# Performance work log

Hardware: AMD Instinct MI355X
Metric: run time of the kernel (lower is better)

The kernel has to match this reference:

```python
import jax, jax.numpy as jnp
import numpy as np

HIDDEN = 1024
HEADS = 16
HEAD_DIM = HIDDEN // HEADS


def setup_inputs() -> dict:
    key = jax.random.key(0)
    k_x, k_wa, k_ba, k_wp, k_bp = jax.random.split(key, 5)
    x = jax.random.normal(k_x, (2, 2048, HIDDEN), dtype=jnp.float32)
    s_a = 1.0 / np.sqrt(HIDDEN)
    # torch Linear default init ~ U(-1/sqrt(fan_in), 1/sqrt(fan_in)); stored as [in, out]
    W_attn = jax.random.uniform(k_wa, (HIDDEN, 3 * HIDDEN), jnp.float32, -s_a, s_a)
    b_attn = jax.random.uniform(k_ba, (3 * HIDDEN,), jnp.float32, -s_a, s_a)
    W_proj = jax.random.uniform(k_wp, (HIDDEN, HIDDEN), jnp.float32, -s_a, s_a)
    b_proj = jax.random.uniform(k_bp, (HIDDEN,), jnp.float32, -s_a, s_a)
    return {"x": x, "W_attn": W_attn, "b_attn": b_attn, "W_proj": W_proj, "b_proj": b_proj}


def reference(x, W_attn, b_attn, W_proj, b_proj):
    B, S, D = x.shape
    H, Hd = HEADS, HEAD_DIM
    qkv = x @ W_attn + b_attn                     # [B, S, 3D]
    q, k, v = jnp.split(qkv, 3, axis=-1)
    # [B, H, S, Hd]
    q = q.reshape(B, S, H, Hd).transpose(0, 2, 1, 3)
    k = k.reshape(B, S, H, Hd).transpose(0, 2, 1, 3)
    v = v.reshape(B, S, H, Hd).transpose(0, 2, 1, 3)
    scale = 1.0 / np.sqrt(Hd).astype(np.float32)
    scores = jnp.einsum('bhqd,bhkd->bhqk', q, k) * scale   # [B, H, S, S]
    causal = jnp.triu(jnp.ones((S, S), dtype=bool), k=1)   # True above diagonal
    scores = jnp.where(causal, -jnp.inf, scores)
    probs = jax.nn.softmax(scores, axis=-1)
    # dropout p=0.0 -> identity (eval-mode equivalent)
    ctx = jnp.einsum('bhqk,bhkd->bhqd', probs, v)           # [B, H, S, Hd]
    ctx = ctx.transpose(0, 2, 1, 3).reshape(B, S, D)
    return ctx @ W_proj + b_proj
```

## Files before the change

### kernel.cpp

```cpp
#include <hip/hip_runtime.h>
#include <hip/hip_bf16.h>
#include <stdint.h>

#define HID 1024
#define NH 16
#define HD 64
#define SEQ 2048
#define BATCH 2
#define M_TOT 4096
#define QSCALE 0.18033688011112042f

typedef __attribute__((ext_vector_type(8))) short short8;
typedef __attribute__((ext_vector_type(4))) float f32x4;
typedef __attribute__((ext_vector_type(16))) float f32x16;
typedef __hip_bfloat16 bf16;

__device__ __forceinline__ void load_lds16(const void* g, void* l) {
  __builtin_amdgcn_global_load_lds(
      (const __attribute__((address_space(1))) unsigned int*)g,
      (__attribute__((address_space(3))) unsigned int*)l, 16, 0, 0);
}

__device__ __forceinline__ unsigned short f2bf_bits(float f) {
  __hip_bfloat16 h = __float2bfloat16(f);
  return *reinterpret_cast<unsigned short*>(&h);
}
__device__ __forceinline__ unsigned pack2bf(float a, float b) {
  return (unsigned)f2bf_bits(a) | ((unsigned)f2bf_bits(b) << 16);
}
__device__ __forceinline__ unsigned cvt_pk_bf16(float a, float b) {
  unsigned r;
  asm("v_cvt_pk_bf16_f32 %0, %1, %2" : "=v"(r) : "v"(a), "v"(b));
  return r;
}

__global__ void cvt_f32_to_bf16(const float* __restrict__ in,
                                bf16* __restrict__ out, int n4) {
  int i = blockIdx.x * blockDim.x + threadIdx.x;
  if (i >= n4) return;
  float4 v = reinterpret_cast<const float4*>(in)[i];
  ushort4 o;
  o.x = f2bf_bits(v.x); o.y = f2bf_bits(v.y);
  o.z = f2bf_bits(v.z); o.w = f2bf_bits(v.w);
  reinterpret_cast<ushort4*>(out)[i] = o;
}

__global__ void transpose_cvt2(const float* __restrict__ Wa, bf16* __restrict__ WTa,
                               const float* __restrict__ Wp, bf16* __restrict__ WTp) {
  __shared__ float tile[32][33];
  int bx = blockIdx.x;
  const float* W; bf16* WT; int N;
  if (bx < 96) { W = Wa; WT = WTa; N = 3072; }
  else         { W = Wp; WT = WTp; N = 1024; bx -= 96; }
  const int K = 1024;
  int n0 = bx * 32, k0 = blockIdx.y * 32;
  int tx = threadIdx.x, ty = threadIdx.y;
#pragma unroll
  for (int i = 0; i < 32; i += 8)
    tile[ty + i][tx] = W[(size_t)(k0 + ty + i) * N + n0 + tx];
  __syncthreads();
#pragma unroll
  for (int i = 0; i < 32; i += 8)
    WT[(size_t)(n0 + ty + i) * K + k0 + tx] = __float2bfloat16(tile[tx][ty + i]);
}

template <int EPI>
__global__ __launch_bounds__(256, 2)
void gemm128(const bf16* __restrict__ A, const bf16* __restrict__ BT,
             const float* __restrict__ bias,
             bf16* __restrict__ Qo, bf16* __restrict__ Ko, bf16* __restrict__ Vo,
             float* __restrict__ Fo) {
  const int Kdim = 1024;
  __shared__ char smem[65536];
  const int tid = threadIdx.x;
  const int wid = tid >> 6, lane = tid & 63;
  const int m0 = blockIdx.x * 128;
  const int n0 = blockIdx.y * 128;
  const int wrow = (wid >> 1) * 64, wcol = (wid & 1) * 64;

  f32x4 acc[4][4];
#pragma unroll
  for (int rb = 0; rb < 4; ++rb)
#pragma unroll
    for (int cb = 0; cb < 4; ++cb)
      acc[rb][cb] = (f32x4){0.f, 0.f, 0.f, 0.f};

  const int lr = lane >> 3;
  const int cc = lane & 7;
  const int lc = cc * 8;
  const int fr = lane & 15, fk = (lane >> 4) * 8;

  auto stage = [&](int kt) {
    char* nb = smem + (kt & 1) * 32768;
#pragma unroll
    for (int t = 0; t < 4; ++t) {
      int i = wid * 4 + t;
      int row = i * 8 + lr;
      load_lds16(A + (size_t)(m0 + row) * Kdim + kt * 64 + lc, nb + i * 1024);
      load_lds16(BT + (size_t)(n0 + row) * Kdim + kt * 64 + lc,
                 nb + 16384 + i * 1024);
    }
  };

  stage(0);

  for (int kt = 0; kt < Kdim / 64; ++kt) {
    const bf16* As = (const bf16*)(smem + (kt & 1) * 32768);
    const bf16* Bs = As + 8192;

    __builtin_amdgcn_s_barrier();
    __builtin_amdgcn_sched_barrier(0);

    if (kt + 1 < Kdim / 64) {
      stage(kt + 1);
      asm volatile("s_waitcnt vmcnt(8)" ::: "memory");
    } else {
      asm volatile("s_waitcnt vmcnt(0)" ::: "memory");
    }
    __builtin_amdgcn_sched_barrier(0);

    __builtin_amdgcn_s_barrier();
    __builtin_amdgcn_sched_barrier(0);

    short8 af[4][2], bf_[4][2];
#pragma unroll
    for (int rb = 0; rb < 4; ++rb)
#pragma unroll
      for (int kk = 0; kk < 2; ++kk) {
        af[rb][kk] = *(const short8*)&As[(wrow + rb * 16 + fr) * 64 + kk * 32 + fk];
        bf_[rb][kk] = *(const short8*)&Bs[(wcol + rb * 16 + fr) * 64 + kk * 32 + fk];
      }
    __builtin_amdgcn_s_setprio(1);
#pragma unroll
    for (int rb = 0; rb < 4; ++rb)
#pragma unroll
      for (int cb = 0; cb < 4; ++cb)
#pragma unroll
        for (int kk = 0; kk < 2; ++kk)
          acc[rb][cb] = __builtin_amdgcn_mfma_f32_16x16x32_bf16(
              af[rb][kk], bf_[cb][kk], acc[rb][cb], 0, 0, 0);
    __builtin_amdgcn_s_setprio(0);
  }

  const int fg = (lane >> 4) * 4;
  float bv[4];
#pragma unroll
  for (int cb = 0; cb < 4; ++cb) bv[cb] = bias[n0 + wcol + cb * 16 + fr];

  if (EPI == 0) {
    __syncthreads();
    char* ep = smem + wid * 8192;
    const int ncol = n0 + wcol;
    const int part = ncol >> 10;
    const int h = (ncol & 1023) >> 6;
    const int b = m0 >> 11;
    const int s_base = (m0 + wrow) & 2047;
    const size_t hb = (size_t)(b * NH + h);

    if (part < 2) {
      const float qs = (part == 0) ? QSCALE : 1.f;
#pragma unroll
      for (int rb = 0; rb < 4; ++rb)
#pragma unroll
        for (int cb = 0; cb < 4; ++cb)
#pragma unroll
          for (int j = 0; j < 4; ++j) {
            int row = rb * 16 + fg + j;
            int colb = (cb * 16 + fr) * 2;
            *(unsigned short*)(ep + row * 128 + (colb ^ ((row & 7) << 4))) =
                f2bf_bits((acc[rb][cb][j] + bv[cb]) * qs);
          }
      bf16* dst = (part == 0 ? Qo : Ko) + hb * SEQ * HD;
#pragma unroll
      for (int p = 0; p < 8; ++p) {
        int row = p * 8 + lr;
        uint4 v = *(const uint4*)(ep + row * 128 + ((cc * 16) ^ ((row & 7) << 4)));
        *(uint4*)(dst + (size_t)(s_base + row) * HD + cc * 8) = v;
      }
    } else {
#pragma unroll
      for (int rb = 0; rb < 4; ++rb)
#pragma unroll
        for (int cb = 0; cb < 4; ++cb) {
          int cV = cb * 16 + fr;
          int r0 = (rb * 16 + fg) * 2;
          uint2 wv;
          wv.x = pack2bf(acc[rb][cb][0] + bv[cb], acc[rb][cb][1] + bv[cb]);
          wv.y = pack2bf(acc[rb][cb][2] + bv[cb], acc[rb][cb][3] + bv[cb]);
          *(uint2*)(ep + cV * 128 + (r0 ^ ((cV & 7) << 4))) = wv;
        }
      bf16* dstV = Vo + hb * HD * SEQ;
#pragma unroll
      for (int p = 0; p < 8; ++p) {
        int hd = p * 8 + lr;
        uint4 v = *(const uint4*)(ep + hd * 128 + ((cc * 16) ^ ((hd & 7) << 4)));
        *(uint4*)(dstV + (size_t)hd * SEQ + s_base + cc * 8) = v;
      }
    }
  } else {
#pragma unroll
    for (int rb = 0; rb < 4; ++rb) {
      int r0 = m0 + wrow + rb * 16 + fg;
#pragma unroll
      for (int cb = 0; cb < 4; ++cb) {
        int n = n0 + wcol + cb * 16 + fr;
#pragma unroll
        for (int j = 0; j < 4; ++j)
          Fo[(size_t)(r0 + j) * HID + n] = acc[rb][cb][j] + bv[cb];
      }
    }
  }
}

__global__ __launch_bounds__(256, 2)
void attn_kernel(const bf16* __restrict__ Q, const bf16* __restrict__ K,
                 const bf16* __restrict__ VT, bf16* __restrict__ ctx) {
  __shared__ char smem[65536];
  const int tid = threadIdx.x, wid = tid >> 6, lane = tid & 63;
  const int idx = blockIdx.x;
  const int qt = (idx < 256) ? (15 - (idx >> 5)) : ((idx - 256) >> 5);
  const int bh = idx & 31;
  const int b = bh >> 4, h = bh & 15;
  const size_t base = (size_t)bh * SEQ * HD;
  const int q0 = qt * 128 + wid * 32;

  const int fr = lane & 31, hi = lane >> 5;
  const int lr = lane >> 3;
  const int cc = lane & 7;
  const int qg = q0 + fr;
  const int gc = (cc ^ lr) * 8;

  short8 qf[4];
  const bf16* qp = Q + base + (size_t)qg * HD;
#pragma unroll
  for (int kc = 0; kc < 4; ++kc)
    qf[kc] = *(const short8*)(qp + kc * 16 + hi * 8);

  f32x16 oa[2], ob[2];
#pragma unroll
  for (int da = 0; da < 2; ++da)
#pragma unroll
    for (int r = 0; r < 16; ++r) { oa[da][r] = 0.f; ob[da][r] = 0.f; }
  float lpart = 0.f;

  auto stage_pair = [&](int jp) {
    char* nb = smem + (jp & 1) * 32768;
    const int nv = jp * 128;
#pragma unroll
    for (int u = 0; u < 2; ++u)
#pragma unroll
      for (int t = 0; t < 2; ++t) {
        int i = wid * 2 + t;
        load_lds16(K + base + (size_t)(nv + u * 64 + i * 8 + lr) * HD + gc,
                   nb + u * 16384 + i * 1024);
        load_lds16(VT + base + (size_t)(i * 8 + lr) * SEQ + nv + u * 64 + gc,
                   nb + u * 16384 + 8192 + i * 1024);
      }
  };

  auto tile_compute = [&](const char* sb_t, int kv0, f32x16 (&oc)[2]) {
    f32x16 sa[2];
    __builtin_amdgcn_s_setprio(1);
#pragma unroll
    for (int kb = 0; kb < 2; ++kb) {
#pragma unroll
      for (int r = 0; r < 16; ++r) sa[kb][r] = 0.f;
      const int row = kb * 32 + fr;
      const int swz = (row & 7) << 4;
#pragma unroll
      for (int kc = 0; kc < 4; ++kc) {
        short8 kf = *(const short8*)(sb_t + row * 128 + ((kc * 32 + hi * 16) ^ swz));
        sa[kb] = __builtin_amdgcn_mfma_f32_32x32x16_bf16(kf, qf[kc], sa[kb], 0, 0, 0);
      }
    }
    __builtin_amdgcn_s_setprio(0);

    if (kv0 + 63 > q0) {
#pragma unroll
      for (int kb = 0; kb < 2; ++kb)
#pragma unroll
        for (int r = 0; r < 16; ++r) {
          int kvg = kv0 + kb * 32 + (r & 3) + 8 * (r >> 2) + 4 * hi;
          sa[kb][r] = (kvg > qg) ? -1e30f : sa[kb][r];
        }
    }

    float s0 = 0.f, s1 = 0.f, s2 = 0.f, s3 = 0.f;
#pragma unroll
    for (int kb = 0; kb < 2; ++kb)
#pragma unroll
      for (int r = 0; r < 16; ++r) {
        float e = __builtin_exp2f(sa[kb][r]);
        sa[kb][r] = e;
        if ((r & 3) == 0)      s0 += e;
        else if ((r & 3) == 1) s1 += e;
        else if ((r & 3) == 2) s2 += e;
        else                   s3 += e;
      }
    lpart += (s0 + s1) + (s2 + s3);

    unsigned pk[2][8];
#pragma unroll
    for (int kb = 0; kb < 2; ++kb)
#pragma unroll
      for (int i = 0; i < 8; ++i)
        pk[kb][i] = cvt_pk_bf16(sa[kb][2 * i], sa[kb][2 * i + 1]);

    short8 pfr[4];
#pragma unroll
    for (int ks = 0; ks < 4; ++ks) {
      const int kb = ks >> 1, g = (ks & 1) * 4;
      auto r0 = __builtin_amdgcn_permlane32_swap((int)pk[kb][g + 0],
                                                 (int)pk[kb][g + 2], false, false);
      auto r1 = __builtin_amdgcn_permlane32_swap((int)pk[kb][g + 1],
                                                 (int)pk[kb][g + 3], false, false);
      union { unsigned u[4]; short8 s; } pf;
      pf.u[0] = (unsigned)r0[0]; pf.u[1] = (unsigned)r1[0];
      pf.u[2] = (unsigned)r0[1]; pf.u[3] = (unsigned)r1[1];
      pfr[ks] = pf.s;
    }

    __builtin_amdgcn_s_setprio(1);
#pragma unroll
    for (int da = 0; da < 2; ++da) {
      const int row = da * 32 + fr;
      const int swz = (row & 7) << 4;
#pragma unroll
      for (int ks = 0; ks < 4; ++ks) {
        short8 vf = *(const short8*)(sb_t + 8192 + row * 128 +
                                     ((ks * 32 + hi * 16) ^ swz));
        oc[da] = __builtin_amdgcn_mfma_f32_32x32x16_bf16(vf, pfr[ks], oc[da], 0, 0, 0);
      }
    }
    __builtin_amdgcn_s_setprio(0);
  };

  const int npair = qt + 1;

  stage_pair(0);

  for (int j = 0; j < npair; ++j) {
    char* sb = smem + (j & 1) * 32768;

    __builtin_amdgcn_s_barrier();
    __builtin_amdgcn_sched_barrier(0);

    if (j + 1 < npair) {
      stage_pair(j + 1);
      asm volatile("s_waitcnt vmcnt(8)" ::: "memory");
    } else {
      asm volatile("s_waitcnt vmcnt(0)" ::: "memory");
    }
    __builtin_amdgcn_sched_barrier(0);

    __builtin_amdgcn_s_barrier();
    __builtin_amdgcn_sched_barrier(0);

    const int kv0 = j * 128;
    if (kv0 <= q0 + 31)      tile_compute(sb,         kv0,      oa);
    if (kv0 + 64 <= q0 + 31) tile_compute(sb + 16384, kv0 + 64, ob);
  }

  const float lrun = lpart + __shfl_xor(lpart, 32);
  const float inv = 1.f / lrun;
  char* ep = smem + wid * 4096;
#pragma unroll
  for (int da = 0; da < 2; ++da)
#pragma unroll
    for (int rg = 0; rg < 4; ++rg) {
      int d0 = da * 64 + rg * 16 + hi * 8;
      float v0 = (oa[da][rg * 4 + 0] + ob[da][rg * 4 + 0]) * inv;
      float v1 = (oa[da][rg * 4 + 1] + ob[da][rg * 4 + 1]) * inv;
      float v2 = (oa[da][rg * 4 + 2] + ob[da][rg * 4 + 2]) * inv;
      float v3 = (oa[da][rg * 4 + 3] + ob[da][rg * 4 + 3]) * inv;
      uint2 wv; wv.x = pack2bf(v0, v1); wv.y = pack2bf(v2, v3);
      *(uint2*)(ep + fr * 128 + (d0 ^ ((fr & 7) << 4))) = wv;
    }
#pragma unroll
  for (int p = 0; p < 4; ++p) {
    int qr = p * 8 + lr;
    uint4 v = *(const uint4*)(ep + qr * 128 + ((cc * 16) ^ ((qr & 7) << 4)));
    int s = q0 + qr;
    *(uint4*)(ctx + (size_t)(b * SEQ + s) * HID + h * 64 + cc * 8) = v;
  }
}

extern "C" void kernel_launch(void* const* d_in, const int* in_sizes, int n_in,
                              void* d_out, int out_size, void* d_ws, size_t ws_size,
                              hipStream_t stream) {
  const float* x      = (const float*)d_in[0];
  const float* W_attn = (const float*)d_in[1];
  const float* b_attn = (const float*)d_in[2];
  const float* W_proj = (const float*)d_in[3];
  const float* b_proj = (const float*)d_in[4];
  float* out = (float*)d_out;

  char* ws = (char*)d_ws;
  const size_t MB = 1u << 20;
  bf16* xb   = (bf16*)(ws + 0);
  bf16* WTa  = (bf16*)(ws + 8 * MB);
  bf16* WTp  = (bf16*)(ws + 14 * MB);
  bf16* Qw   = (bf16*)(ws + 16 * MB);
  bf16* Kw   = (bf16*)(ws + 24 * MB);
  bf16* VTw  = (bf16*)(ws + 32 * MB);
  bf16* ctxb = (bf16*)(ws + 40 * MB);

  cvt_f32_to_bf16<<<(M_TOT * HID / 4 + 255) / 256, 256, 0, stream>>>(x, xb, M_TOT * HID / 4);
  transpose_cvt2<<<dim3(128, 32), dim3(32, 8), 0, stream>>>(W_attn, WTa, W_proj, WTp);

  gemm128<0><<<dim3(M_TOT / 128, 3 * HID / 128), 256, 0, stream>>>(
      xb, WTa, b_attn, Qw, Kw, VTw, nullptr);

  attn_kernel<<<dim3(512), 256, 0, stream>>>(Qw, Kw, VTw, ctxb);

  gemm128<1><<<dim3(M_TOT / 128, HID / 128), 256, 0, stream>>>(
      ctxb, WTp, b_proj, nullptr, nullptr, nullptr, out);
}
```

Before: 108.6 us.

## Swizzle GEMM LDS tiles and fuse prep kernels into one launch

Applies an XOR swizzle to the chunk positions of the A and B tiles staged in LDS and matches it in the fragment reads, to reduce LDS bank conflicts in the bf16 MFMA GEMMs. It also merges the x conversion and weight transpose-convert kernels into a single launch with a flattened 1D grid, removing one kernel launch. The cost is more index arithmetic per block.

```diff
diff --git a/kernel.cpp b/kernel.cpp
--- a/kernel.cpp
+++ b/kernel.cpp
@@ -34,27 +34,27 @@
   return r;
 }
 
-__global__ void cvt_f32_to_bf16(const float* __restrict__ in,
-                                bf16* __restrict__ out, int n4) {
-  int i = blockIdx.x * blockDim.x + threadIdx.x;
-  if (i >= n4) return;
-  float4 v = reinterpret_cast<const float4*>(in)[i];
-  ushort4 o;
-  o.x = f2bf_bits(v.x); o.y = f2bf_bits(v.y);
-  o.z = f2bf_bits(v.z); o.w = f2bf_bits(v.w);
-  reinterpret_cast<ushort4*>(out)[i] = o;
-}
-
-__global__ void transpose_cvt2(const float* __restrict__ Wa, bf16* __restrict__ WTa,
-                               const float* __restrict__ Wp, bf16* __restrict__ WTp) {
+__global__ void prep_all(const float* __restrict__ x, bf16* __restrict__ xb,
+                         const float* __restrict__ Wa, bf16* __restrict__ WTa,
+                         const float* __restrict__ Wp, bf16* __restrict__ WTp) {
   __shared__ float tile[32][33];
   int bx = blockIdx.x;
-  const float* W; bf16* WT; int N;
-  if (bx < 96) { W = Wa; WT = WTa; N = 3072; }
-  else         { W = Wp; WT = WTp; N = 1024; bx -= 96; }
+  if (bx < 4096) {
+    int i = bx * 256 + threadIdx.x;
+    float4 v = reinterpret_cast<const float4*>(x)[i];
+    ushort4 o;
+    o.x = f2bf_bits(v.x); o.y = f2bf_bits(v.y);
+    o.z = f2bf_bits(v.z); o.w = f2bf_bits(v.w);
+    reinterpret_cast<ushort4*>(xb)[i] = o;
+    return;
+  }
+  bx -= 4096;
+  const float* W; bf16* WT; int N, tpr;
+  if (bx < 3072) { W = Wa; WT = WTa; N = 3072; tpr = 96; }
+  else           { W = Wp; WT = WTp; N = 1024; tpr = 32; bx -= 3072; }
   const int K = 1024;
-  int n0 = bx * 32, k0 = blockIdx.y * 32;
-  int tx = threadIdx.x, ty = threadIdx.y;
+  int n0 = (bx % tpr) * 32, k0 = (bx / tpr) * 32;
+  int tx = threadIdx.x & 31, ty = threadIdx.x >> 5;
 #pragma unroll
   for (int i = 0; i < 32; i += 8)
     tile[ty + i][tx] = W[(size_t)(k0 + ty + i) * N + n0 + tx];
@@ -87,8 +87,10 @@
 
   const int lr = lane >> 3;
   const int cc = lane & 7;
-  const int lc = cc * 8;
-  const int fr = lane & 15, fk = (lane >> 4) * 8;
+  const int gc = (cc ^ lr) * 8;
+  const int fr = lane & 15;
+  const int fk2 = (lane >> 4) * 16;
+  const int fswz = (fr & 7) << 4;
 
   auto stage = [&](int kt) {
     char* nb = smem + (kt & 1) * 32768;
@@ -96,8 +98,8 @@
     for (int t = 0; t < 4; ++t) {
       int i = wid * 4 + t;
       int row = i * 8 + lr;
-      load_lds16(A + (size_t)(m0 + row) * Kdim + kt * 64 + lc, nb + i * 1024);
-      load_lds16(BT + (size_t)(n0 + row) * Kdim + kt * 64 + lc,
+      load_lds16(A + (size_t)(m0 + row) * Kdim + kt * 64 + gc, nb + i * 1024);
+      load_lds16(BT + (size_t)(n0 + row) * Kdim + kt * 64 + gc,
                  nb + 16384 + i * 1024);
     }
   };
@@ -105,8 +107,8 @@
   stage(0);
 
   for (int kt = 0; kt < Kdim / 64; ++kt) {
-    const bf16* As = (const bf16*)(smem + (kt & 1) * 32768);
-    const bf16* Bs = As + 8192;
+    const char* Asc = smem + (kt & 1) * 32768;
+    const char* Bsc = Asc + 16384;
 
     __builtin_amdgcn_s_barrier();
     __builtin_amdgcn_sched_barrier(0);
@@ -127,8 +129,10 @@
     for (int rb = 0; rb < 4; ++rb)
 #pragma unroll
       for (int kk = 0; kk < 2; ++kk) {
-        af[rb][kk] = *(const short8*)&As[(wrow + rb * 16 + fr) * 64 + kk * 32 + fk];
-        bf_[rb][kk] = *(const short8*)&Bs[(wcol + rb * 16 + fr) * 64 + kk * 32 + fk];
+        af[rb][kk] = *(const short8*)(Asc + (wrow + rb * 16 + fr) * 128 +
+                                      ((kk * 64 + fk2) ^ fswz));
+        bf_[rb][kk] = *(const short8*)(Bsc + (wcol + rb * 16 + fr) * 128 +
+                                       ((kk * 64 + fk2) ^ fswz));
       }
     __builtin_amdgcn_s_setprio(1);
 #pragma unroll
@@ -405,8 +409,7 @@
   bf16* VTw  = (bf16*)(ws + 32 * MB);
   bf16* ctxb = (bf16*)(ws + 40 * MB);
 
-  cvt_f32_to_bf16<<<(M_TOT * HID / 4 + 255) / 256, 256, 0, stream>>>(x, xb, M_TOT * HID / 4);
-  transpose_cvt2<<<dim3(128, 32), dim3(32, 8), 0, stream>>>(W_attn, WTa, W_proj, WTp);
+  prep_all<<<dim3(8192), 256, 0, stream>>>(x, xb, W_attn, WTa, W_proj, WTp);
 
   gemm128<0><<<dim3(M_TOT / 128, 3 * HID / 128), 256, 0, stream>>>(
       xb, WTa, b_attn, Qw, Kw, VTw, nullptr);
```

Result: faster. 98.03 us (-9.7%).
